# Kernel optimization log

Measured on AMD Instinct MI355X. Metric: run time of the kernel, lower is better.

## Reference

```python
import jax, jax.numpy as jnp
import numpy as np

B, S, D, H = 4, 2048, 1024, 16
HD = D // H


def setup_inputs() -> dict:
    key = jax.random.key(0)
    ks = jax.random.split(key, 6)
    scale = 1.0 / np.sqrt(D)
    return {
        'x': jax.random.normal(ks[0], (B, S, D), dtype=jnp.float32),
        'wq': jax.random.normal(ks[1], (D, D), dtype=jnp.float32) * scale,
        'wk': jax.random.normal(ks[2], (D, D), dtype=jnp.float32) * scale,
        'wv': jax.random.normal(ks[3], (D, D), dtype=jnp.float32) * scale,
        'wo': jax.random.normal(ks[4], (D, D), dtype=jnp.float32) * scale,
        'wo_b': jnp.zeros((D,), dtype=jnp.float32),
    }


def reference(x, wq, wk, wv, wo, wo_b):
    b, s, _ = x.shape
    # Linear projections (torch Linear: x @ W.T), reshape to [b, h, s, hd]
    def proj(w):
        return jnp.einsum('bsd,ed->bse', x, w).reshape(b, s, H, HD).transpose(0, 2, 1, 3)
    q, k, v = proj(wq), proj(wk), proj(wv)
    scores = jnp.einsum('bhqd,bhkd->bhqk', q, k)  # [b,h,s,s]
    causal = jnp.triu(jnp.ones((s, s), dtype=bool), k=1)
    scores = jnp.where(causal, -jnp.inf, scores)
    attn = jax.nn.softmax(scores / np.sqrt(HD), axis=-1)
    ctx = jnp.einsum('bhqk,bhkd->bhqd', attn, v)  # [b,h,s,hd]
    ctx = ctx.transpose(0, 2, 1, 3).reshape(b, s, D)
    return jnp.einsum('bsd,ed->bse', ctx, wo) + wo_b
```

## Files before the change

kernel.cpp:

```cpp
#include <hip/hip_runtime.h>

#define SB 4
#define SS 2048
#define SD 1024
#define SH 16
#define SHD 64
#define SM (SB * SS)

typedef __bf16 bf16x8 __attribute__((ext_vector_type(8)));
typedef float f32x4 __attribute__((ext_vector_type(4)));

static __device__ __forceinline__ unsigned short f2bf(float x) {
    unsigned int u = __builtin_bit_cast(unsigned int, x);
    u += 0x7fffu + ((u >> 16) & 1u);
    return (unsigned short)(u >> 16);
}

static __device__ __forceinline__ float fast_exp2(float x) {
#if __has_builtin(__builtin_amdgcn_exp2f)
    return __builtin_amdgcn_exp2f(x);
#else
    return exp2f(x);
#endif
}

static __device__ __forceinline__ unsigned int pkhi(float a, float b) {
    return __builtin_amdgcn_perm(__builtin_bit_cast(unsigned int, a),
                                 __builtin_bit_cast(unsigned int, b), 0x07060302u);
}

typedef __attribute__((address_space(1))) void GV;
typedef __attribute__((address_space(3))) void LV;

static __device__ __forceinline__ void async16(const void* g, void* l) {
    __builtin_amdgcn_global_load_lds((GV*)g, (LV*)l, 16, 0, 0);
}

#define QSCALE 0.18033688011112042f

__global__ __launch_bounds__(256) void cast_all(
    const float* __restrict__ x,  const float* __restrict__ wq,
    const float* __restrict__ wk, const float* __restrict__ wv,
    const float* __restrict__ wo,
    unsigned short* __restrict__ xb, unsigned short* __restrict__ wqkv,
    unsigned short* __restrict__ wo16) {
    int i = blockIdx.x * 256 + threadIdx.x;
    const float4* src;
    ushort4* dst;
    if (i < 2097152) {
        src = reinterpret_cast<const float4*>(x) + i;
        dst = reinterpret_cast<ushort4*>(xb) + i;
    } else {
        int j = i - 2097152;
        int which = j >> 18;
        int r = j & 262143;
        const float* ws_[4] = {wq, wk, wv, wo};
        src = reinterpret_cast<const float4*>(ws_[which]) + r;
        dst = (which < 3 ? reinterpret_cast<ushort4*>(wqkv) + which * 262144
                         : reinterpret_cast<ushort4*>(wo16)) + r;
    }
    float4 v = *src;
    ushort4 o;
    o.x = f2bf(v.x); o.y = f2bf(v.y); o.z = f2bf(v.z); o.w = f2bf(v.w);
    *dst = o;
}

__device__ __forceinline__ void gemm128_compute(
    const unsigned short* __restrict__ Asc,
    const unsigned short* __restrict__ Bsc,
    int wr, int wc, int col0, int fchunk, f32x4 (&acc)[4][4]) {
    bf16x8 af[4], bfr[4];
#pragma unroll
    for (int rt = 0; rt < 4; ++rt)
        af[rt] = *reinterpret_cast<const bf16x8*>(
            Asc + (wr * 64 + rt * 16 + col0) * 32 + fchunk);
#pragma unroll
    for (int ct = 0; ct < 4; ++ct)
        bfr[ct] = *reinterpret_cast<const bf16x8*>(
            Bsc + (wc * 64 + ct * 16 + col0) * 32 + fchunk);
#pragma unroll
    for (int rt = 0; rt < 4; ++rt)
#pragma unroll
        for (int ct = 0; ct < 4; ++ct)
            acc[rt][ct] = __builtin_amdgcn_mfma_f32_16x16x32_bf16(
                af[rt], bfr[ct], acc[rt][ct], 0, 0, 0);
}

__device__ __forceinline__ void gemm128_mainloop(
    const unsigned short* __restrict__ A,
    const unsigned short* __restrict__ Bt,
    int tileM, int tileN, int tid,
    unsigned short* As0, unsigned short* Bs0,
    unsigned short* As1, unsigned short* Bs1,
    f32x4 (&acc)[4][4]) {

    const int lane = tid & 63;
    const int quad = lane >> 4;
    const int col0 = lane & 15;
    const int wr = tid >> 7;
    const int wc = (tid >> 6) & 1;

    const int srow = tid >> 2;
    const int schunk = ((tid & 3) ^ (srow & 3)) * 8;
    const unsigned short* Ab = A + (size_t)(tileM + srow) * SD + schunk;
    const unsigned short* Bb = Bt + (size_t)(tileN + srow) * SD + schunk;
    const size_t rowskip = (size_t)64 * SD;

    char* As0D = (char*)As0 + tid * 16;
    char* Bs0D = (char*)Bs0 + tid * 16;
    char* As1D = (char*)As1 + tid * 16;
    char* Bs1D = (char*)Bs1 + tid * 16;

    const int fchunk = (quad ^ (col0 & 3)) * 8;

    async16(Ab, As0D);
    async16(Ab + rowskip, As0D + 4096);
    async16(Bb, Bs0D);
    async16(Bb + rowskip, Bs0D + 4096);

#pragma unroll 1
    for (int kt = 0; kt < 32; kt += 2) {
        const int ke = (kt + 1) << 5;
        __syncthreads();
        async16(Ab + ke, As1D);
        async16(Ab + ke + rowskip, As1D + 4096);
        async16(Bb + ke, Bs1D);
        async16(Bb + ke + rowskip, Bs1D + 4096);
        gemm128_compute(As0, Bs0, wr, wc, col0, fchunk, acc);

        __syncthreads();
        if (kt < 30) {
            const int ko = (kt + 2) << 5;
            async16(Ab + ko, As0D);
            async16(Ab + ko + rowskip, As0D + 4096);
            async16(Bb + ko, Bs0D);
            async16(Bb + ko + rowskip, Bs0D + 4096);
        }
        gemm128_compute(As1, Bs1, wr, wc, col0, fchunk, acc);
    }
}

__global__ __launch_bounds__(256) void gemm_qkv(
    const unsigned short* __restrict__ xb,
    const unsigned short* __restrict__ wqkv,
    unsigned short* __restrict__ Qd,
    unsigned short* __restrict__ Kd,
    unsigned short* __restrict__ Vtd) {

    __shared__ __align__(16) unsigned short As0[128 * 32];
    __shared__ __align__(16) unsigned short Bs0[128 * 32];
    __shared__ __align__(16) unsigned short As1[128 * 32];
    __shared__ __align__(16) unsigned short Bs1[128 * 32];
    const int tid = threadIdx.x;
    const int tileN = blockIdx.x * 128;
    const int tileM = blockIdx.y * 128;

    f32x4 acc[4][4];
    const f32x4 z = {0.f, 0.f, 0.f, 0.f};
#pragma unroll
    for (int i = 0; i < 4; ++i)
#pragma unroll
        for (int j = 0; j < 4; ++j) acc[i][j] = z;

    gemm128_mainloop(xb, wqkv, tileM, tileN, tid, As0, Bs0, As1, Bs1, acc);

    const int lane = tid & 63, quad = lane >> 4, col0 = lane & 15;
    const int wr = tid >> 7, wc = (tid >> 6) & 1;

#pragma unroll
    for (int ct = 0; ct < 4; ++ct) {
        int n0 = tileN + wc * 64 + ct * 16;
        int which = n0 >> 10;
        int e0 = n0 & 1023;
        int h = e0 >> 6;
        int hd = (e0 & 63) + col0;
#pragma unroll
        for (int rt = 0; rt < 4; ++rt) {
            int m0 = tileM + wr * 64 + rt * 16 + quad * 4;
            int bb = m0 >> 11;
            int s0 = m0 & 2047;
            int bh = bb * SH + h;
            if (which == 0) {
                int base = (bh * SS + s0) * SHD + hd;
#pragma unroll
                for (int r = 0; r < 4; ++r)
                    Qd[base + r * SHD] = f2bf(acc[rt][ct][r] * QSCALE);
            } else if (which == 1) {
                int base = (bh * SS + s0) * SHD + hd;
#pragma unroll
                for (int r = 0; r < 4; ++r)
                    Kd[base + r * SHD] = f2bf(acc[rt][ct][r]);
            } else {
                int base = (bh * SHD + hd) * SS + s0;
                ushort4 pk;
                pk.x = f2bf(acc[rt][ct][0]);
                pk.y = f2bf(acc[rt][ct][1]);
                pk.z = f2bf(acc[rt][ct][2]);
                pk.w = f2bf(acc[rt][ct][3]);
                *reinterpret_cast<ushort4*>(Vtd + base) = pk;
            }
        }
    }
}

__global__ __launch_bounds__(256) void gemm_out(
    const unsigned short* __restrict__ ctx,
    const unsigned short* __restrict__ wo16,
    const float* __restrict__ wb,
    float* __restrict__ out) {

    __shared__ __align__(16) unsigned short As0[128 * 32];
    __shared__ __align__(16) unsigned short Bs0[128 * 32];
    __shared__ __align__(16) unsigned short As1[128 * 32];
    __shared__ __align__(16) unsigned short Bs1[128 * 32];
    const int tid = threadIdx.x;
    const int tileN = blockIdx.x * 128;
    const int tileM = blockIdx.y * 128;

    f32x4 acc[4][4];
    const f32x4 z = {0.f, 0.f, 0.f, 0.f};
#pragma unroll
    for (int i = 0; i < 4; ++i)
#pragma unroll
        for (int j = 0; j < 4; ++j) acc[i][j] = z;

    gemm128_mainloop(ctx, wo16, tileM, tileN, tid, As0, Bs0, As1, Bs1, acc);

    const int lane = tid & 63, quad = lane >> 4, col0 = lane & 15;
    const int wr = tid >> 7, wc = (tid >> 6) & 1;

#pragma unroll
    for (int ct = 0; ct < 4; ++ct) {
        int n = tileN + wc * 64 + ct * 16 + col0;
        float bias = wb[n];
#pragma unroll
        for (int rt = 0; rt < 4; ++rt) {
            int m0 = tileM + wr * 64 + rt * 16 + quad * 4;
#pragma unroll
            for (int r = 0; r < 4; ++r)
                out[(size_t)(m0 + r) * SD + n] = acc[rt][ct][r] + bias;
        }
    }
}

#define PSTR 72

__device__ __forceinline__ void attn_pass(
    const unsigned short* __restrict__ Qg,
    const unsigned short* __restrict__ Kg,
    const unsigned short* __restrict__ Vtg,
    unsigned short* __restrict__ ctx,
    size_t base, int b, int h, int jj,
    int tid, int w, int quad, int col0,
    unsigned short* Ks0, unsigned short* Ks1,
    unsigned short* Vs0, unsigned short* Vs1,
    unsigned short* Psw, const bf16x8& ones) {

    const int q0 = jj * 128 + w * 32;

    bf16x8 bq[2][2];
#pragma unroll
    for (int g = 0; g < 2; ++g)
#pragma unroll
        for (int ks = 0; ks < 2; ++ks)
            bq[g][ks] = *reinterpret_cast<const bf16x8*>(
                Qg + base + (size_t)(q0 + g * 16 + col0) * SHD + ks * 32 + quad * 8);

    f32x4 ot[2][4], lacc[2];
    const f32x4 z = {0.f, 0.f, 0.f, 0.f};
#pragma unroll
    for (int g = 0; g < 2; ++g) {
        lacc[g] = z;
#pragma unroll
        for (int ct = 0; ct < 4; ++ct) ot[g][ct] = z;
    }

    const int srow0 = tid >> 3;
    const int scs = tid & 7;

    unsigned short* KsB[2] = {Ks0, Ks1};
    unsigned short* VsB[2] = {Vs0, Vs1};

    const int nkt = 2 * jj + 2;

    __syncthreads();
#pragma unroll
    for (int j = 0; j < 2; ++j) {
        int row = j * 32 + srow0;
        int chunk = scs ^ (row & 7);
        int slot16 = (j * 256 + tid) * 16;
        async16(Kg + base + (size_t)row * SHD + chunk * 8, (char*)Ks0 + slot16);
        async16(Vtg + base + (size_t)row * SS + chunk * 8, (char*)Vs0 + slot16);
    }

    for (int kt = 0; kt < nkt; ++kt) {
        const int kb = kt * 64;
        __syncthreads();

        if (kt + 1 < nkt) {
            const int kb1 = kb + 64;
            unsigned short* Kn = KsB[(kt + 1) & 1];
            unsigned short* Vn = VsB[(kt + 1) & 1];
#pragma unroll
            for (int j = 0; j < 2; ++j) {
                int row = j * 32 + srow0;
                int chunk = scs ^ (row & 7);
                int slot16 = (j * 256 + tid) * 16;
                async16(Kg + base + (size_t)(kb1 + row) * SHD + chunk * 8,
                        (char*)Kn + slot16);
                async16(Vtg + base + (size_t)row * SS + kb1 + chunk * 8,
                        (char*)Vn + slot16);
            }
        }

        if (kb > q0 + 31) continue;

        const unsigned short* Kc = KsB[kt & 1];
        const unsigned short* Vc = VsB[kt & 1];

        bf16x8 ak[4][2];
#pragma unroll
        for (int rt = 0; rt < 4; ++rt)
#pragma unroll
            for (int ks = 0; ks < 2; ++ks)
                ak[rt][ks] = *reinterpret_cast<const bf16x8*>(
                    &Kc[(rt * 16 + col0) * 64 + ((ks * 4 + quad) ^ (col0 & 7)) * 8]);

        f32x4 sc[2][4];
#pragma unroll
        for (int g = 0; g < 2; ++g)
#pragma unroll
            for (int rt = 0; rt < 4; ++rt) sc[g][rt] = z;
#pragma unroll
        for (int rt = 0; rt < 4; ++rt)
#pragma unroll
            for (int g = 0; g < 2; ++g) {
                sc[g][rt] = __builtin_amdgcn_mfma_f32_16x16x32_bf16(
                    ak[rt][0], bq[g][0], sc[g][rt], 0, 0, 0);
                sc[g][rt] = __builtin_amdgcn_mfma_f32_16x16x32_bf16(
                    ak[rt][1], bq[g][1], sc[g][rt], 0, 0, 0);
            }

        if (kb + 63 > q0) {
#pragma unroll
            for (int g = 0; g < 2; ++g) {
                int q = q0 + g * 16 + col0;
#pragma unroll
                for (int rt = 0; rt < 4; ++rt)
#pragma unroll
                    for (int r = 0; r < 4; ++r) {
                        int key = kb + rt * 16 + quad * 4 + r;
                        if (key > q) sc[g][rt][r] = -3.0e38f;
                    }
            }
        }

#pragma unroll
        for (int g = 0; g < 2; ++g)
#pragma unroll
            for (int rt = 0; rt < 4; ++rt)
#pragma unroll
                for (int r = 0; r < 4; ++r)
                    sc[g][rt][r] = fast_exp2(sc[g][rt][r]);

#pragma unroll
        for (int g = 0; g < 2; ++g) {
            unsigned short* Pw = Psw + g * 16 * PSTR;
#pragma unroll
            for (int rt = 0; rt < 4; ++rt) {
                uint2 pk;
                pk.x = pkhi(sc[g][rt][1], sc[g][rt][0]);
                pk.y = pkhi(sc[g][rt][3], sc[g][rt][2]);
                *reinterpret_cast<uint2*>(&Pw[col0 * PSTR + rt * 16 + quad * 4]) = pk;
            }
        }

#pragma unroll
        for (int ks = 0; ks < 2; ++ks) {
            bf16x8 bp[2];
#pragma unroll
            for (int g = 0; g < 2; ++g) {
                bp[g] = *reinterpret_cast<const bf16x8*>(
                    &Psw[g * 16 * PSTR + col0 * PSTR + ks * 32 + quad * 8]);
                lacc[g] = __builtin_amdgcn_mfma_f32_16x16x32_bf16(
                    ones, bp[g], lacc[g], 0, 0, 0);
            }
#pragma unroll
            for (int ct = 0; ct < 4; ++ct) {
                bf16x8 av = *reinterpret_cast<const bf16x8*>(
                    &Vc[(ct * 16 + col0) * 64 + ((ks * 4 + quad) ^ (col0 & 7)) * 8]);
#pragma unroll
                for (int g = 0; g < 2; ++g)
                    ot[g][ct] = __builtin_amdgcn_mfma_f32_16x16x32_bf16(
                        av, bp[g], ot[g][ct], 0, 0, 0);
            }
        }
    }

#pragma unroll
    for (int g = 0; g < 2; ++g) {
        float inv = 1.0f / lacc[g][0];
        int q = q0 + g * 16 + col0;
        size_t obase = ((size_t)b * SS + q) * SD + h * SHD;
#pragma unroll
        for (int ct = 0; ct < 4; ++ct) {
            uint2 pk;
            pk.x = pkhi(ot[g][ct][1] * inv, ot[g][ct][0] * inv);
            pk.y = pkhi(ot[g][ct][3] * inv, ot[g][ct][2] * inv);
            *reinterpret_cast<uint2*>(ctx + obase + ct * 16 + quad * 4) = pk;
        }
    }
}

__global__ __launch_bounds__(256) void attn_kernel(
    const unsigned short* __restrict__ Qg,
    const unsigned short* __restrict__ Kg,
    const unsigned short* __restrict__ Vtg,
    unsigned short* __restrict__ ctx) {

    __shared__ __align__(16) unsigned short Ks0[64 * 64];
    __shared__ __align__(16) unsigned short Ks1[64 * 64];
    __shared__ __align__(16) unsigned short Vs0[64 * 64];
    __shared__ __align__(16) unsigned short Vs1[64 * 64];
    __shared__ __align__(16) unsigned short Ps[8 * 16 * PSTR];

    const int tid = threadIdx.x;
    const int w = tid >> 6;
    const int lane = tid & 63;
    const int quad = lane >> 4;
    const int col0 = lane & 15;
    const int bh = blockIdx.y;
    const int b = bh >> 4;
    const int h = bh & 15;
    const size_t base = (size_t)bh * (SS * SHD);
    unsigned short* Psw = Ps + w * 2 * 16 * PSTR;

    bf16x8 ones;
#pragma unroll
    for (int i = 0; i < 8; ++i) ones[i] = (__bf16)1.0f;

    attn_pass(Qg, Kg, Vtg, ctx, base, b, h, blockIdx.x,
              tid, w, quad, col0, Ks0, Ks1, Vs0, Vs1, Psw, ones);
    attn_pass(Qg, Kg, Vtg, ctx, base, b, h, 15 - blockIdx.x,
              tid, w, quad, col0, Ks0, Ks1, Vs0, Vs1, Psw, ones);
}

extern "C" void kernel_launch(void* const* d_in, const int* in_sizes, int n_in,
                              void* d_out, int out_size, void* d_ws, size_t ws_size,
                              hipStream_t stream) {
    const float* x  = (const float*)d_in[0];
    const float* wq = (const float*)d_in[1];
    const float* wk = (const float*)d_in[2];
    const float* wv = (const float*)d_in[3];
    const float* wo = (const float*)d_in[4];
    const float* wb = (const float*)d_in[5];
    float* out = (float*)d_out;

    char* ws = (char*)d_ws;
    unsigned short* xb   = (unsigned short*)(ws + 0);
    unsigned short* wqkv = (unsigned short*)(ws + 16777216);
    unsigned short* q    = (unsigned short*)(ws + 23068672);
    unsigned short* k    = (unsigned short*)(ws + 39845888);
    unsigned short* vt   = (unsigned short*)(ws + 56623104);
    unsigned short* ctx  = (unsigned short*)(ws + 73400320);
    unsigned short* wo16 = (unsigned short*)(ws + 90177536);

    cast_all<<<12288, 256, 0, stream>>>(x, wq, wk, wv, wo, xb, wqkv, wo16);

    gemm_qkv<<<dim3(3 * SD / 128, SM / 128), 256, 0, stream>>>(xb, wqkv, q, k, vt);

    attn_kernel<<<dim3(8, SB * SH), 256, 0, stream>>>(q, k, vt, ctx);

    gemm_out<<<dim3(SD / 128, SM / 128), 256, 0, stream>>>(ctx, wo16, wb, out);
}
```

Measured before the change: 262.0 us.

## Process two KV tiles per barrier with four-buffer K/V staging in attention

The attention inner loop now uses four K/V shared-memory buffers and handles two 64-key tiles between each pair of barriers. The next two tiles are prefetched while the current two are computed, which halves the number of __syncthreads per key and deepens the prefetch distance. The P scratch buffer shrinks to one 16-row slab per wave, reused across the two query groups. In exchange, LDS use rises from about 46KB to about 73KB per block, which may lower occupancy.

```diff
diff --git a/kernel.cpp b/kernel.cpp
--- a/kernel.cpp
+++ b/kernel.cpp
@@ -245,6 +245,107 @@
 
 #define PSTR 72
 
+__device__ __forceinline__ void stage_kv(
+    const unsigned short* __restrict__ Kg,
+    const unsigned short* __restrict__ Vtg,
+    size_t base, int t, int srow0, int scs, int tid,
+    unsigned short* Kb, unsigned short* Vb) {
+#pragma unroll
+    for (int j = 0; j < 2; ++j) {
+        int row = j * 32 + srow0;
+        int chunk = scs ^ (row & 7);
+        int slot16 = (j * 256 + tid) * 16;
+        async16(Kg + base + (size_t)(t * 64 + row) * SHD + chunk * 8,
+                (char*)Kb + slot16);
+        async16(Vtg + base + (size_t)row * SS + t * 64 + chunk * 8,
+                (char*)Vb + slot16);
+    }
+}
+
+__device__ __forceinline__ void attn_tile(
+    const unsigned short* __restrict__ Kc,
+    const unsigned short* __restrict__ Vc,
+    int kb, int q0, int quad, int col0,
+    const bf16x8 (&bq)[2][2], const bf16x8& ones,
+    unsigned short* Psw, f32x4 (&ot)[2][4], f32x4 (&lacc)[2]) {
+
+    const f32x4 z = {0.f, 0.f, 0.f, 0.f};
+
+    bf16x8 ak[4][2];
+#pragma unroll
+    for (int rt = 0; rt < 4; ++rt)
+#pragma unroll
+        for (int ks = 0; ks < 2; ++ks)
+            ak[rt][ks] = *reinterpret_cast<const bf16x8*>(
+                &Kc[(rt * 16 + col0) * 64 + ((ks * 4 + quad) ^ (col0 & 7)) * 8]);
+
+    f32x4 sc[2][4];
+#pragma unroll
+    for (int g = 0; g < 2; ++g)
+#pragma unroll
+        for (int rt = 0; rt < 4; ++rt) sc[g][rt] = z;
+#pragma unroll
+    for (int rt = 0; rt < 4; ++rt)
+#pragma unroll
+        for (int g = 0; g < 2; ++g) {
+            sc[g][rt] = __builtin_amdgcn_mfma_f32_16x16x32_bf16(
+                ak[rt][0], bq[g][0], sc[g][rt], 0, 0, 0);
+            sc[g][rt] = __builtin_amdgcn_mfma_f32_16x16x32_bf16(
+                ak[rt][1], bq[g][1], sc[g][rt], 0, 0, 0);
+        }
+
+    if (kb + 63 > q0) {
+#pragma unroll
+        for (int g = 0; g < 2; ++g) {
+            int q = q0 + g * 16 + col0;
+#pragma unroll
+            for (int rt = 0; rt < 4; ++rt)
+#pragma unroll
+                for (int r = 0; r < 4; ++r) {
+                    int key = kb + rt * 16 + quad * 4 + r;
+                    if (key > q) sc[g][rt][r] = -3.0e38f;
+                }
+        }
+    }
+
+#pragma unroll
+    for (int g = 0; g < 2; ++g)
+#pragma unroll
+        for (int rt = 0; rt < 4; ++rt)
+#pragma unroll
+            for (int r = 0; r < 4; ++r)
+                sc[g][rt][r] = fast_exp2(sc[g][rt][r]);
+
+    bf16x8 bp[2][2];
+#pragma unroll
+    for (int g = 0; g < 2; ++g) {
+#pragma unroll
+        for (int rt = 0; rt < 4; ++rt) {
+            uint2 pk;
+            pk.x = pkhi(sc[g][rt][1], sc[g][rt][0]);
+            pk.y = pkhi(sc[g][rt][3], sc[g][rt][2]);
+            *reinterpret_cast<uint2*>(&Psw[col0 * PSTR + rt * 16 + quad * 4]) = pk;
+        }
+#pragma unroll
+        for (int ks = 0; ks < 2; ++ks)
+            bp[g][ks] = *reinterpret_cast<const bf16x8*>(
+                &Psw[col0 * PSTR + ks * 32 + quad * 8]);
+    }
+
+#pragma unroll
+    for (int ks = 0; ks < 2; ++ks) {
+        lacc[0] = __builtin_amdgcn_mfma_f32_16x16x32_bf16(ones, bp[0][ks], lacc[0], 0, 0, 0);
+        lacc[1] = __builtin_amdgcn_mfma_f32_16x16x32_bf16(ones, bp[1][ks], lacc[1], 0, 0, 0);
+#pragma unroll
+        for (int ct = 0; ct < 4; ++ct) {
+            bf16x8 av = *reinterpret_cast<const bf16x8*>(
+                &Vc[(ct * 16 + col0) * 64 + ((ks * 4 + quad) ^ (col0 & 7)) * 8]);
+            ot[0][ct] = __builtin_amdgcn_mfma_f32_16x16x32_bf16(av, bp[0][ks], ot[0][ct], 0, 0, 0);
+            ot[1][ct] = __builtin_amdgcn_mfma_f32_16x16x32_bf16(av, bp[1][ks], ot[1][ct], 0, 0, 0);
+        }
+    }
+}
+
 __device__ __forceinline__ void attn_pass(
     const unsigned short* __restrict__ Qg,
     const unsigned short* __restrict__ Kg,
@@ -252,11 +353,12 @@
     unsigned short* __restrict__ ctx,
     size_t base, int b, int h, int jj,
     int tid, int w, int quad, int col0,
-    unsigned short* Ks0, unsigned short* Ks1,
-    unsigned short* Vs0, unsigned short* Vs1,
+    unsigned short* K0, unsigned short* K1, unsigned short* K2, unsigned short* K3,
+    unsigned short* V0, unsigned short* V1, unsigned short* V2, unsigned short* V3,
     unsigned short* Psw, const bf16x8& ones) {
 
     const int q0 = jj * 128 + w * 32;
+    const int qlim = q0 + 31;
 
     bf16x8 bq[2][2];
 #pragma unroll
@@ -277,124 +379,30 @@
 
     const int srow0 = tid >> 3;
     const int scs = tid & 7;
-
-    unsigned short* KsB[2] = {Ks0, Ks1};
-    unsigned short* VsB[2] = {Vs0, Vs1};
-
     const int nkt = 2 * jj + 2;
 
     __syncthreads();
-#pragma unroll
-    for (int j = 0; j < 2; ++j) {
-        int row = j * 32 + srow0;
-        int chunk = scs ^ (row & 7);
-        int slot16 = (j * 256 + tid) * 16;
-        async16(Kg + base + (size_t)row * SHD + chunk * 8, (char*)Ks0 + slot16);
-        async16(Vtg + base + (size_t)row * SS + chunk * 8, (char*)Vs0 + slot16);
-    }
-
-    for (int kt = 0; kt < nkt; ++kt) {
-        const int kb = kt * 64;
+    stage_kv(Kg, Vtg, base, 0, srow0, scs, tid, K0, V0);
+    if (1 < nkt) stage_kv(Kg, Vtg, base, 1, srow0, scs, tid, K1, V1);
+
+#pragma unroll 1
+    for (int kt = 0; kt < nkt; kt += 4) {
         __syncthreads();
-
-        if (kt + 1 < nkt) {
-            const int kb1 = kb + 64;
-            unsigned short* Kn = KsB[(kt + 1) & 1];
-            unsigned short* Vn = VsB[(kt + 1) & 1];
-#pragma unroll
-            for (int j = 0; j < 2; ++j) {
-                int row = j * 32 + srow0;
-                int chunk = scs ^ (row & 7);
-                int slot16 = (j * 256 + tid) * 16;
-                async16(Kg + base + (size_t)(kb1 + row) * SHD + chunk * 8,
-                        (char*)Kn + slot16);
-                async16(Vtg + base + (size_t)row * SS + kb1 + chunk * 8,
-                        (char*)Vn + slot16);
-            }
-        }
-
-        if (kb > q0 + 31) continue;
-
-        const unsigned short* Kc = KsB[kt & 1];
-        const unsigned short* Vc = VsB[kt & 1];
-
-        bf16x8 ak[4][2];
-#pragma unroll
-        for (int rt = 0; rt < 4; ++rt)
-#pragma unroll
-            for (int ks = 0; ks < 2; ++ks)
-                ak[rt][ks] = *reinterpret_cast<const bf16x8*>(
-                    &Kc[(rt * 16 + col0) * 64 + ((ks * 4 + quad) ^ (col0 & 7)) * 8]);
-
-        f32x4 sc[2][4];
-#pragma unroll
-        for (int g = 0; g < 2; ++g)
-#pragma unroll
-            for (int rt = 0; rt < 4; ++rt) sc[g][rt] = z;
-#pragma unroll
-        for (int rt = 0; rt < 4; ++rt)
-#pragma unroll
-            for (int g = 0; g < 2; ++g) {
-                sc[g][rt] = __builtin_amdgcn_mfma_f32_16x16x32_bf16(
-                    ak[rt][0], bq[g][0], sc[g][rt], 0, 0, 0);
-                sc[g][rt] = __builtin_amdgcn_mfma_f32_16x16x32_bf16(
-                    ak[rt][1], bq[g][1], sc[g][rt], 0, 0, 0);
-            }
-
-        if (kb + 63 > q0) {
-#pragma unroll
-            for (int g = 0; g < 2; ++g) {
-                int q = q0 + g * 16 + col0;
-#pragma unroll
-                for (int rt = 0; rt < 4; ++rt)
-#pragma unroll
-                    for (int r = 0; r < 4; ++r) {
-                        int key = kb + rt * 16 + quad * 4 + r;
-                        if (key > q) sc[g][rt][r] = -3.0e38f;
-                    }
-            }
-        }
-
-#pragma unroll
-        for (int g = 0; g < 2; ++g)
-#pragma unroll
-            for (int rt = 0; rt < 4; ++rt)
-#pragma unroll
-                for (int r = 0; r < 4; ++r)
-                    sc[g][rt][r] = fast_exp2(sc[g][rt][r]);
-
-#pragma unroll
-        for (int g = 0; g < 2; ++g) {
-            unsigned short* Pw = Psw + g * 16 * PSTR;
-#pragma unroll
-            for (int rt = 0; rt < 4; ++rt) {
-                uint2 pk;
-                pk.x = pkhi(sc[g][rt][1], sc[g][rt][0]);
-                pk.y = pkhi(sc[g][rt][3], sc[g][rt][2]);
-                *reinterpret_cast<uint2*>(&Pw[col0 * PSTR + rt * 16 + quad * 4]) = pk;
-            }
-        }
-
-#pragma unroll
-        for (int ks = 0; ks < 2; ++ks) {
-            bf16x8 bp[2];
-#pragma unroll
-            for (int g = 0; g < 2; ++g) {
-                bp[g] = *reinterpret_cast<const bf16x8*>(
-                    &Psw[g * 16 * PSTR + col0 * PSTR + ks * 32 + quad * 8]);
-                lacc[g] = __builtin_amdgcn_mfma_f32_16x16x32_bf16(
-                    ones, bp[g], lacc[g], 0, 0, 0);
-            }
-#pragma unroll
-            for (int ct = 0; ct < 4; ++ct) {
-                bf16x8 av = *reinterpret_cast<const bf16x8*>(
-                    &Vc[(ct * 16 + col0) * 64 + ((ks * 4 + quad) ^ (col0 & 7)) * 8]);
-#pragma unroll
-                for (int g = 0; g < 2; ++g)
-                    ot[g][ct] = __builtin_amdgcn_mfma_f32_16x16x32_bf16(
-                        av, bp[g], ot[g][ct], 0, 0, 0);
-            }
-        }
+        if (kt + 2 < nkt) stage_kv(Kg, Vtg, base, kt + 2, srow0, scs, tid, K2, V2);
+        if (kt + 3 < nkt) stage_kv(Kg, Vtg, base, kt + 3, srow0, scs, tid, K3, V3);
+        if (kt * 64 <= qlim)
+            attn_tile(K0, V0, kt * 64, q0, quad, col0, bq, ones, Psw, ot, lacc);
+        if ((kt + 1) * 64 <= qlim)
+            attn_tile(K1, V1, (kt + 1) * 64, q0, quad, col0, bq, ones, Psw, ot, lacc);
+
+        if (kt + 2 >= nkt) break;
+        __syncthreads();
+        if (kt + 4 < nkt) stage_kv(Kg, Vtg, base, kt + 4, srow0, scs, tid, K0, V0);
+        if (kt + 5 < nkt) stage_kv(Kg, Vtg, base, kt + 5, srow0, scs, tid, K1, V1);
+        if ((kt + 2) * 64 <= qlim)
+            attn_tile(K2, V2, (kt + 2) * 64, q0, quad, col0, bq, ones, Psw, ot, lacc);
+        if (kt + 3 < nkt && (kt + 3) * 64 <= qlim)
+            attn_tile(K3, V3, (kt + 3) * 64, q0, quad, col0, bq, ones, Psw, ot, lacc);
     }
 
 #pragma unroll
@@ -418,11 +426,15 @@
     const unsigned short* __restrict__ Vtg,
     unsigned short* __restrict__ ctx) {
 
-    __shared__ __align__(16) unsigned short Ks0[64 * 64];
-    __shared__ __align__(16) unsigned short Ks1[64 * 64];
-    __shared__ __align__(16) unsigned short Vs0[64 * 64];
-    __shared__ __align__(16) unsigned short Vs1[64 * 64];
-    __shared__ __align__(16) unsigned short Ps[8 * 16 * PSTR];
+    __shared__ __align__(16) unsigned short K0[64 * 64];
+    __shared__ __align__(16) unsigned short K1[64 * 64];
+    __shared__ __align__(16) unsigned short K2[64 * 64];
+    __shared__ __align__(16) unsigned short K3[64 * 64];
+    __shared__ __align__(16) unsigned short V0[64 * 64];
+    __shared__ __align__(16) unsigned short V1[64 * 64];
+    __shared__ __align__(16) unsigned short V2[64 * 64];
+    __shared__ __align__(16) unsigned short V3[64 * 64];
+    __shared__ __align__(16) unsigned short Ps[4 * 16 * PSTR];
 
     const int tid = threadIdx.x;
     const int w = tid >> 6;
@@ -433,16 +445,16 @@
     const int b = bh >> 4;
     const int h = bh & 15;
     const size_t base = (size_t)bh * (SS * SHD);
-    unsigned short* Psw = Ps + w * 2 * 16 * PSTR;
+    unsigned short* Psw = Ps + w * 16 * PSTR;
 
     bf16x8 ones;
 #pragma unroll
     for (int i = 0; i < 8; ++i) ones[i] = (__bf16)1.0f;
 
     attn_pass(Qg, Kg, Vtg, ctx, base, b, h, blockIdx.x,
-              tid, w, quad, col0, Ks0, Ks1, Vs0, Vs1, Psw, ones);
+              tid, w, quad, col0, K0, K1, K2, K3, V0, V1, V2, V3, Psw, ones);
     attn_pass(Qg, Kg, Vtg, ctx, base, b, h, 15 - blockIdx.x,
-              tid, w, quad, col0, Ks0, Ks1, Vs0, Vs1, Psw, ones);
+              tid, w, quad, col0, K0, K1, K2, K3, V0, V1, V2, V3, Psw, ones);
 }
 
 extern "C" void kernel_launch(void* const* d_in, const int* in_sizes, int n_in,
```

Result: faster. 250.0 us (-4.6%).
